# Kernel optimization log

Measured on AMD Instinct MI355X. Metric: run time of the kernel, lower is better.

## Reference

```python
import jax, jax.numpy as jnp
import numpy as np

N, E, D, L = 50000, 800000, 128, 3

def setup_inputs() -> dict:
    key = jax.random.key(0)
    ks = jax.random.split(key, 6)
    X = jax.random.normal(ks[0], (N, D), dtype=jnp.float32)
    edge_index = jax.random.randint(ks[1], (2, E), 0, N, dtype=jnp.int64)
    eps = jax.random.normal(ks[2], (L,), dtype=jnp.float32)
    # Glorot-ish scaling for stability
    W1 = jax.random.normal(ks[3], (L, D, D), dtype=jnp.float32) / np.sqrt(D)
    b1 = jnp.zeros((L, D), dtype=jnp.float32)
    W2 = jax.random.normal(ks[4], (L, D, D), dtype=jnp.float32) / np.sqrt(D)
    b2 = jnp.zeros((L, D), dtype=jnp.float32)
    return {"X": X, "edge_index": edge_index, "eps": eps,
            "W1": W1, "b1": b1, "W2": W2, "b2": b2}

def reference(X, edge_index, eps, W1, b1, W2, b2):
    src = edge_index[0]  # message sources j (flow source_to_target)
    dst = edge_index[1]  # aggregation targets i
    n = X.shape[0]
    for i in range(L):  # fixed small layer loop
        X0 = X
        # propagate: gather X_j over edges, scatter-add to targets
        S = jax.ops.segment_sum(X[src], dst, num_segments=n)  # [N, D]
        Z = (1.0 + eps[i]) * X + S
        # MLP: Linear -> ReLU -> Linear
        H = jnp.maximum(Z @ W1[i] + b1[i], 0.0)
        X = H @ W2[i] + b2[i]
        X = X + X0  # residual=True
    return X
```

## Files before the change

### kernel.cpp

```cpp
#include <hip/hip_runtime.h>

#define NN 50000
#define NE 800000
#define DD 128
#define NL 3
#define ELLW 96
#define MT_TOTAL (NN / 16)

typedef short bf16x8 __attribute__((ext_vector_type(8)));
typedef float f32x4 __attribute__((ext_vector_type(4)));
typedef _Float16 half8 __attribute__((ext_vector_type(8)));

__device__ __forceinline__ unsigned short f2bf(float x) {
  unsigned u = __float_as_uint(x);
  u += 0x7FFFu + ((u >> 16) & 1u);
  return (unsigned short)(u >> 16);
}
__device__ __forceinline__ float bf2f(unsigned short h) {
  return __uint_as_float(((unsigned)h) << 16);
}
__device__ __forceinline__ void cvt8(float4 z0, float4 z1, bf16x8* hi, bf16x8* lo) {
  float zz[8] = {z0.x, z0.y, z0.z, z0.w, z1.x, z1.y, z1.z, z1.w};
#pragma unroll
  for (int i = 0; i < 8; ++i) {
    unsigned short h = f2bf(zz[i]);
    (*hi)[i] = (short)h;
    (*lo)[i] = (short)f2bf(zz[i] - bf2f(h));
  }
}

__global__ __launch_bounds__(256) void build_ell_k(const int* __restrict__ ei,
                                                   int* __restrict__ cnt,
                                                   int* __restrict__ ell) {
  int e = blockIdx.x * 256 + threadIdx.x;
  if (e >= NE) return;
  int s = ei[e];
  int d = ei[NE + e];
  int pos = atomicAdd(&cnt[d], 1);
  if (pos < ELLW) ell[(size_t)d * ELLW + pos] = s;
}

__global__ __launch_bounds__(256) void pack_w_k(const float* __restrict__ W1,
                                                const float* __restrict__ W2,
                                                unsigned short* __restrict__ Wp) {
  int t = blockIdx.x * 256 + threadIdx.x;
  if (t >= 6 * 2048) return;
  int m = t >> 11;
  int rem = t & 2047;
  int l = rem & 63;
  int ntks = rem >> 6;
  int ks = ntks & 3, nt = ntks >> 2;
  const float* W = (m < 3) ? (W1 + (size_t)m * DD * DD) : (W2 + (size_t)(m - 3) * DD * DD);
  int col = nt * 16 + (l & 15);
  int k0 = ks * 32 + (l >> 4) * 8;
  unsigned short* hi = Wp + (size_t)m * 2 * DD * DD + (size_t)rem * 8;
  unsigned short* lo = hi + DD * DD;
#pragma unroll
  for (int i = 0; i < 8; ++i) {
    float w = W[(size_t)(k0 + i) * DD + col];
    unsigned short h = f2bf(w);
    hi[i] = h;
    lo[i] = f2bf(w - bf2f(h));
  }
}

__global__ __launch_bounds__(256) void xh_init_k(const float* __restrict__ X,
                                                 _Float16* __restrict__ Xh) {
  int t = blockIdx.x * 256 + threadIdx.x;
  if (t >= NN * DD / 8) return;
  const float4* p = (const float4*)X + (size_t)t * 2;
  float4 a = p[0], b = p[1];
  half8 h;
  h[0] = (_Float16)a.x; h[1] = (_Float16)a.y; h[2] = (_Float16)a.z; h[3] = (_Float16)a.w;
  h[4] = (_Float16)b.x; h[5] = (_Float16)b.y; h[6] = (_Float16)b.z; h[7] = (_Float16)b.w;
  *(half8*)(Xh + (size_t)t * 8) = h;
}

template<int WRITE_H>
__global__ __launch_bounds__(256) void fused_layer_k(
    const float* __restrict__ Xf_in, const _Float16* __restrict__ Xh_in,
    const int* __restrict__ cnt, const int* __restrict__ ell,
    const float* __restrict__ eps, int layer,
    const unsigned short* __restrict__ Wp1, const float* __restrict__ b1,
    const unsigned short* __restrict__ Wp2, const float* __restrict__ b2,
    float* __restrict__ Xf_out, _Float16* __restrict__ Xh_out)
{
  __shared__ float tile[2][16 * 132];
  const int w = threadIdx.x >> 6, l = threadIdx.x & 63;
  const int pair = w >> 1, h = w & 1;
  const int mt = blockIdx.x * 2 + pair;
  const bool active = (mt < MT_TOTAL);
  const int c = l & 15, grp = l >> 4;
  float* my = tile[pair];

  if (active) {
    const float e1 = 1.0f + eps[layer];
#pragma unroll
    for (int pass = 0; pass < 2; ++pass) {
      int nl = h * 8 + pass * 4 + grp;
      int node = mt * 16 + nl;
      int deg = cnt[node]; deg = deg > ELLW ? ELLW : deg;
      const int* el = ell + (size_t)node * ELLW;
      const int4* el4 = (const int4*)el;
      float acc[8];
      {
        const float* xr = Xf_in + (size_t)node * DD + c * 8;
        float4 a0 = *(const float4*)xr, a1 = *(const float4*)(xr + 4);
        acc[0] = e1 * a0.x; acc[1] = e1 * a0.y; acc[2] = e1 * a0.z; acc[3] = e1 * a0.w;
        acc[4] = e1 * a1.x; acc[5] = e1 * a1.y; acc[6] = e1 * a1.z; acc[7] = e1 * a1.w;
      }
      int nf = deg >> 2;
      int4 nxt;
      if (nf) nxt = el4[0];
      for (int t = 0; t < nf; ++t) {
        int4 cur = nxt;
        if (t + 1 < nf) nxt = el4[t + 1];
        half8 v0 = *(const half8*)(Xh_in + (size_t)cur.x * DD + c * 8);
        half8 v1 = *(const half8*)(Xh_in + (size_t)cur.y * DD + c * 8);
        half8 v2 = *(const half8*)(Xh_in + (size_t)cur.z * DD + c * 8);
        half8 v3 = *(const half8*)(Xh_in + (size_t)cur.w * DD + c * 8);
#pragma unroll
        for (int i = 0; i < 8; ++i)
          acc[i] += ((float)v0[i] + (float)v1[i]) + ((float)v2[i] + (float)v3[i]);
      }
      for (int j = nf * 4; j < deg; ++j) {
        half8 v = *(const half8*)(Xh_in + (size_t)el[j] * DD + c * 8);
#pragma unroll
        for (int i = 0; i < 8; ++i) acc[i] += (float)v[i];
      }
      float* dst = my + nl * 132 + c * 8;
      *(float4*)dst = make_float4(acc[0], acc[1], acc[2], acc[3]);
      *(float4*)(dst + 4) = make_float4(acc[4], acc[5], acc[6], acc[7]);
    }
  }
  __syncthreads();

  f32x4 acc1[4];
#pragma unroll
  for (int nt = 0; nt < 4; ++nt) acc1[nt] = (f32x4){0.f, 0.f, 0.f, 0.f};
  if (active) {
    const float* arow = my + (l & 15) * 132;
    const unsigned short* Whi = Wp1;
    const unsigned short* Wlo = Wp1 + DD * DD;
#pragma unroll
    for (int ks = 0; ks < 4; ++ks) {
      const float* zp = arow + ks * 32 + grp * 8;
      float4 z0 = *(const float4*)zp, z1 = *(const float4*)(zp + 4);
      bf16x8 ahi, alo; cvt8(z0, z1, &ahi, &alo);
#pragma unroll
      for (int nt = 0; nt < 4; ++nt) {
        int ntb = h * 4 + nt;
        size_t off = ((size_t)(ntb * 4 + ks) * 64 + l) * 8;
        bf16x8 bhi = *(const bf16x8*)(Whi + off);
        bf16x8 blo = *(const bf16x8*)(Wlo + off);
        acc1[nt] = __builtin_amdgcn_mfma_f32_16x16x32_bf16(ahi, bhi, acc1[nt], 0, 0, 0);
        acc1[nt] = __builtin_amdgcn_mfma_f32_16x16x32_bf16(ahi, blo, acc1[nt], 0, 0, 0);
        acc1[nt] = __builtin_amdgcn_mfma_f32_16x16x32_bf16(alo, bhi, acc1[nt], 0, 0, 0);
      }
    }
  }
  __syncthreads();

  if (active) {
#pragma unroll
    for (int nt = 0; nt < 4; ++nt) {
      int ntb = h * 4 + nt;
      float bv = b1[ntb * 16 + c];
#pragma unroll
      for (int r = 0; r < 4; ++r)
        my[(grp * 4 + r) * 132 + ntb * 16 + c] = fmaxf(acc1[nt][r] + bv, 0.f);
    }
  }
  __syncthreads();

  f32x4 acc2[4];
#pragma unroll
  for (int nt = 0; nt < 4; ++nt) acc2[nt] = (f32x4){0.f, 0.f, 0.f, 0.f};
  if (active) {
    const float* arow = my + (l & 15) * 132;
    const unsigned short* Whi = Wp2;
    const unsigned short* Wlo = Wp2 + DD * DD;
#pragma unroll
    for (int ks = 0; ks < 4; ++ks) {
      const float* hp = arow + ks * 32 + grp * 8;
      float4 h0 = *(const float4*)hp, h1 = *(const float4*)(hp + 4);
      bf16x8 ahi, alo; cvt8(h0, h1, &ahi, &alo);
#pragma unroll
      for (int nt = 0; nt < 4; ++nt) {
        int ntb = h * 4 + nt;
        size_t off = ((size_t)(ntb * 4 + ks) * 64 + l) * 8;
        bf16x8 bhi = *(const bf16x8*)(Whi + off);
        bf16x8 blo = *(const bf16x8*)(Wlo + off);
        acc2[nt] = __builtin_amdgcn_mfma_f32_16x16x32_bf16(ahi, bhi, acc2[nt], 0, 0, 0);
        acc2[nt] = __builtin_amdgcn_mfma_f32_16x16x32_bf16(ahi, blo, acc2[nt], 0, 0, 0);
        acc2[nt] = __builtin_amdgcn_mfma_f32_16x16x32_bf16(alo, bhi, acc2[nt], 0, 0, 0);
      }
    }
#pragma unroll
    for (int nt = 0; nt < 4; ++nt) {
      int ntb = h * 4 + nt;
      int col = ntb * 16 + c;
      float bv = b2[col];
#pragma unroll
      for (int r = 0; r < 4; ++r) {
        int node = mt * 16 + grp * 4 + r;
        size_t idx = (size_t)node * DD + col;
        float v = acc2[nt][r] + bv + Xf_in[idx];
        Xf_out[idx] = v;
        if (WRITE_H) Xh_out[idx] = (_Float16)v;
      }
    }
  }
}

extern "C" void kernel_launch(void* const* d_in, const int* in_sizes, int n_in,
                              void* d_out, int out_size, void* d_ws, size_t ws_size,
                              hipStream_t stream) {
  const float* X   = (const float*)d_in[0];
  const int*   ei  = (const int*)d_in[1];
  const float* eps = (const float*)d_in[2];
  const float* W1  = (const float*)d_in[3];
  const float* b1  = (const float*)d_in[4];
  const float* W2  = (const float*)d_in[5];
  const float* b2  = (const float*)d_in[6];
  float* Xout = (float*)d_out;

  char* ws = (char*)d_ws;
  size_t off = 0;
  int* cnt = (int*)(ws + off); off += 256 * (((size_t)NN * 4 + 255) / 256);
  int* ell = (int*)(ws + off); off += (size_t)NN * ELLW * 4;
  unsigned short* Wp = (unsigned short*)(ws + off); off += (size_t)6 * 2 * DD * DD * 2;
  _Float16* Xh0 = (_Float16*)(ws + off); off += (size_t)NN * DD * 2;
  _Float16* Xh1 = (_Float16*)(ws + off); off += (size_t)NN * DD * 2;

  hipMemsetAsync(cnt, 0, NN * 4, stream);
  build_ell_k<<<(NE + 255) / 256, 256, 0, stream>>>(ei, cnt, ell);
  pack_w_k<<<(6 * 2048 + 255) / 256, 256, 0, stream>>>(W1, W2, Wp);
  xh_init_k<<<(NN * DD / 8 + 255) / 256, 256, 0, stream>>>(X, Xh0);

  const int fgrid = (MT_TOTAL + 1) / 2;
  fused_layer_k<1><<<fgrid, 256, 0, stream>>>(X, Xh0, cnt, ell, eps, 0,
      Wp + (size_t)0 * 2 * DD * DD, b1 + 0 * DD,
      Wp + (size_t)3 * 2 * DD * DD, b2 + 0 * DD, Xout, Xh1);
  fused_layer_k<1><<<fgrid, 256, 0, stream>>>(Xout, Xh1, cnt, ell, eps, 1,
      Wp + (size_t)1 * 2 * DD * DD, b1 + 1 * DD,
      Wp + (size_t)4 * 2 * DD * DD, b2 + 1 * DD, Xout, Xh0);
  fused_layer_k<0><<<fgrid, 256, 0, stream>>>(Xout, Xh0, cnt, ell, eps, 2,
      Wp + (size_t)2 * 2 * DD * DD, b1 + 2 * DD,
      Wp + (size_t)5 * 2 * DD * DD, b2 + 2 * DD, Xout, nullptr);
}
```

Baseline: 224.4 us.

## Cache residual rows in LDS, use nontemporal loads/stores, shrink ELL width

The self rows loaded for the aggregation step are kept in a second LDS tile, and the residual add in the epilogue reads them from there instead of re-reading Xf_in from global memory. Self-row loads, ELL index loads and the output stores now use nontemporal builtins so they pollute the cache less and leave room for the gathered neighbour rows. ELLW drops from 96 to 64, which shrinks the ELL buffer. Any node with more than 64 in-edges is silently truncated, so correctness depends on the random graph's maximum degree. The extra LDS tile also raises shared memory use per block.

Measured after the change: 236.9 us. 5.6% more time.

```diff
diff --git a/kernel.cpp b/kernel.cpp
--- a/kernel.cpp
+++ b/kernel.cpp
@@ -4,12 +4,14 @@
 #define NE 800000
 #define DD 128
 #define NL 3
-#define ELLW 96
+#define ELLW 64
 #define MT_TOTAL (NN / 16)
 
 typedef short bf16x8 __attribute__((ext_vector_type(8)));
 typedef float f32x4 __attribute__((ext_vector_type(4)));
 typedef _Float16 half8 __attribute__((ext_vector_type(8)));
+typedef int i32x4 __attribute__((ext_vector_type(4)));
+typedef float f32x4v __attribute__((ext_vector_type(4)));
 
 __device__ __forceinline__ unsigned short f2bf(float x) {
   unsigned u = __float_as_uint(x);
@@ -85,13 +87,15 @@
     const unsigned short* __restrict__ Wp2, const float* __restrict__ b2,
     float* __restrict__ Xf_out, _Float16* __restrict__ Xh_out)
 {
-  __shared__ float tile[2][16 * 132];
+  __shared__ float ztile[2][16 * 132];
+  __shared__ float rtile[2][16 * 130];
   const int w = threadIdx.x >> 6, l = threadIdx.x & 63;
   const int pair = w >> 1, h = w & 1;
   const int mt = blockIdx.x * 2 + pair;
   const bool active = (mt < MT_TOTAL);
   const int c = l & 15, grp = l >> 4;
-  float* my = tile[pair];
+  float* my = ztile[pair];
+  float* rz = rtile[pair];
 
   if (active) {
     const float e1 = 1.0f + eps[layer];
@@ -101,30 +105,40 @@
       int node = mt * 16 + nl;
       int deg = cnt[node]; deg = deg > ELLW ? ELLW : deg;
       const int* el = ell + (size_t)node * ELLW;
-      const int4* el4 = (const int4*)el;
+      const i32x4* el4 = (const i32x4*)el;
       float acc[8];
+      float selfv[8];
       {
-        const float* xr = Xf_in + (size_t)node * DD + c * 8;
-        float4 a0 = *(const float4*)xr, a1 = *(const float4*)(xr + 4);
-        acc[0] = e1 * a0.x; acc[1] = e1 * a0.y; acc[2] = e1 * a0.z; acc[3] = e1 * a0.w;
-        acc[4] = e1 * a1.x; acc[5] = e1 * a1.y; acc[6] = e1 * a1.z; acc[7] = e1 * a1.w;
+        const f32x4v* xr = (const f32x4v*)(Xf_in + (size_t)node * DD + c * 8);
+        f32x4v a0 = __builtin_nontemporal_load(xr);
+        f32x4v a1 = __builtin_nontemporal_load(xr + 1);
+#pragma unroll
+        for (int i = 0; i < 4; ++i) { selfv[i] = a0[i]; selfv[4 + i] = a1[i]; }
+#pragma unroll
+        for (int i = 0; i < 8; ++i) acc[i] = e1 * selfv[i];
+      }
+      {
+        float* rd = rz + nl * 130 + c * 8;
+#pragma unroll
+        for (int i = 0; i < 8; ++i) rd[i] = selfv[i];
       }
       int nf = deg >> 2;
-      int4 nxt;
-      if (nf) nxt = el4[0];
+      i32x4 nxt;
+      if (nf) nxt = __builtin_nontemporal_load(el4);
       for (int t = 0; t < nf; ++t) {
-        int4 cur = nxt;
-        if (t + 1 < nf) nxt = el4[t + 1];
-        half8 v0 = *(const half8*)(Xh_in + (size_t)cur.x * DD + c * 8);
-        half8 v1 = *(const half8*)(Xh_in + (size_t)cur.y * DD + c * 8);
-        half8 v2 = *(const half8*)(Xh_in + (size_t)cur.z * DD + c * 8);
-        half8 v3 = *(const half8*)(Xh_in + (size_t)cur.w * DD + c * 8);
+        i32x4 cur = nxt;
+        if (t + 1 < nf) nxt = __builtin_nontemporal_load(el4 + t + 1);
+        half8 v0 = *(const half8*)(Xh_in + (size_t)cur[0] * DD + c * 8);
+        half8 v1 = *(const half8*)(Xh_in + (size_t)cur[1] * DD + c * 8);
+        half8 v2 = *(const half8*)(Xh_in + (size_t)cur[2] * DD + c * 8);
+        half8 v3 = *(const half8*)(Xh_in + (size_t)cur[3] * DD + c * 8);
 #pragma unroll
         for (int i = 0; i < 8; ++i)
           acc[i] += ((float)v0[i] + (float)v1[i]) + ((float)v2[i] + (float)v3[i]);
       }
       for (int j = nf * 4; j < deg; ++j) {
-        half8 v = *(const half8*)(Xh_in + (size_t)el[j] * DD + c * 8);
+        int s = __builtin_nontemporal_load(el + j);
+        half8 v = *(const half8*)(Xh_in + (size_t)s * DD + c * 8);
 #pragma unroll
         for (int i = 0; i < 8; ++i) acc[i] += (float)v[i];
       }
@@ -203,11 +217,12 @@
       float bv = b2[col];
 #pragma unroll
       for (int r = 0; r < 4; ++r) {
-        int node = mt * 16 + grp * 4 + r;
+        int row = grp * 4 + r;
+        int node = mt * 16 + row;
         size_t idx = (size_t)node * DD + col;
-        float v = acc2[nt][r] + bv + Xf_in[idx];
-        Xf_out[idx] = v;
-        if (WRITE_H) Xh_out[idx] = (_Float16)v;
+        float v = acc2[nt][r] + bv + rz[row * 130 + col];
+        __builtin_nontemporal_store(v, Xf_out + idx);
+        if (WRITE_H) __builtin_nontemporal_store((_Float16)v, Xh_out + idx);
       }
     }
   }
```
